# Optimization experiments

Hardware: AMD Instinct MI355X
Metric: run time of the kernel (lower is better)

## Reference

```python
import jax, jax.numpy as jnp
import numpy as np

NEIGHBOR_N = 3


def setup_inputs() -> dict:
    key = jax.random.key(0)
    ks = jax.random.split(key, 4)
    B, D = 8192, 512
    H = D // 2
    sess_emb = jax.random.normal(ks[0], (B, D), dtype=jnp.float32)
    pool_emb = jax.random.normal(ks[1], (1024, D), dtype=jnp.float32)
    # torch Linear default init ~ U(-1/sqrt(fan_in), 1/sqrt(fan_in)); scaled normals ok as baseline
    W1 = jax.random.normal(ks[2], (D, H), dtype=jnp.float32) / np.sqrt(D)
    b1 = jnp.zeros((H,), dtype=jnp.float32)
    W2 = jax.random.normal(ks[3], (H, D), dtype=jnp.float32) / np.sqrt(H)
    b2 = jnp.zeros((D,), dtype=jnp.float32)
    return {"sess_emb": sess_emb, "pool_emb": pool_emb, "W1": W1, "b1": b1, "W2": W2, "b2": b2}


def reference(sess_emb, pool_emb, W1, b1, W2, b2):
    # scoring MLP (dropout = identity in eval mode)
    h = jax.nn.relu(sess_emb @ W1 + b1)          # (B, D/2)
    sess_proj = h @ W2 + b2                       # (B, D)
    # self-similarity and top-k neighbors
    sim_matrix = sess_proj @ sess_proj.T          # (B, B)
    cos_topk, topk_indice = jax.lax.top_k(sim_matrix, NEIGHBOR_N)  # (B, K)
    sess_topk = sess_emb[topk_indice]             # (B, K, D) gather
    cos_topk = jax.nn.softmax(cos_topk, axis=-1)  # (B, K)
    neighbor_sess = jnp.einsum('bk,bkd->bd', cos_topk, sess_topk)  # (B, D)
    return (sess_topk, neighbor_sess, cos_topk)
```

## Files before the change

### kernel.cpp

```cpp
#include <hip/hip_runtime.h>
#include <hip/hip_bf16.h>
#include <math.h>

#define NB 8192
#define DD 512
#define HH 256
#define BM 128
#define BN 256
#define BK 32
#define KT (DD / BK)
#define NCT (NB / BN)
#define NCAND 8

typedef unsigned short ushortT;
typedef __attribute__((ext_vector_type(8))) short bf16x8;
typedef __attribute__((ext_vector_type(4))) float f32x4;

#define AS1(p) ((const __attribute__((address_space(1))) void*)(p))
#define AS3(p) ((__attribute__((address_space(3))) void*)(p))

__device__ __forceinline__ ushortT bf16rne(float f) {
    unsigned u = __float_as_uint(f);
    unsigned r = u + 0x7FFFu + ((u >> 16) & 1u);
    return (ushortT)(r >> 16);
}
__device__ __forceinline__ float bf16tof(ushortT h) {
    return __uint_as_float(((unsigned)h) << 16);
}

__global__ __launch_bounds__(256)
void prep_kernel(const float* __restrict__ sess, const float* __restrict__ W1,
                 const float* __restrict__ W2,
                 ushortT* __restrict__ sess_hi, ushortT* __restrict__ sess_lo,
                 ushortT* __restrict__ w1t_hi, ushortT* __restrict__ w1t_lo,
                 ushortT* __restrict__ w2t_hi, ushortT* __restrict__ w2t_lo) {
    const int b = blockIdx.x, t = threadIdx.x;
    if (b < 2048) {
        size_t i = (size_t)b * 2048 + t * 8;
        float4 f0 = *(const float4*)&sess[i];
        float4 f1 = *(const float4*)&sess[i + 4];
        float f[8] = {f0.x, f0.y, f0.z, f0.w, f1.x, f1.y, f1.z, f1.w};
        unsigned hp[4], lp[4];
#pragma unroll
        for (int j = 0; j < 4; ++j) {
            ushortT h0 = bf16rne(f[2 * j]), h1 = bf16rne(f[2 * j + 1]);
            ushortT l0 = bf16rne(f[2 * j] - bf16tof(h0));
            ushortT l1 = bf16rne(f[2 * j + 1] - bf16tof(h1));
            hp[j] = (unsigned)h0 | ((unsigned)h1 << 16);
            lp[j] = (unsigned)l0 | ((unsigned)l1 << 16);
        }
        *(uint4*)&sess_hi[i] = *(uint4*)hp;
        *(uint4*)&sess_lo[i] = *(uint4*)lp;
    } else if (b < 2112) {
        int o = (b - 2048) * 2048 + t * 8;
        int k = o >> 8, c = o & 255;
        float4 f0 = *(const float4*)&W1[(size_t)k * 256 + c];
        float4 f1 = *(const float4*)&W1[(size_t)k * 256 + c + 4];
        float f[8] = {f0.x, f0.y, f0.z, f0.w, f1.x, f1.y, f1.z, f1.w};
#pragma unroll
        for (int j = 0; j < 8; ++j) {
            ushortT h = bf16rne(f[j]);
            w1t_hi[(size_t)(c + j) * 512 + k] = h;
            w1t_lo[(size_t)(c + j) * 512 + k] = bf16rne(f[j] - bf16tof(h));
        }
    } else {
        int o = (b - 2112) * 2048 + t * 8;
        int k = o >> 9, c = o & 511;
        float4 f0 = *(const float4*)&W2[(size_t)k * 512 + c];
        float4 f1 = *(const float4*)&W2[(size_t)k * 512 + c + 4];
        float f[8] = {f0.x, f0.y, f0.z, f0.w, f1.x, f1.y, f1.z, f1.w};
#pragma unroll
        for (int j = 0; j < 8; ++j) {
            ushortT h = bf16rne(f[j]);
            w2t_hi[(size_t)(c + j) * 256 + k] = h;
            w2t_lo[(size_t)(c + j) * 256 + k] = bf16rne(f[j] - bf16tof(h));
        }
    }
}

template <int KDIM, int NOUT, int EPI>
__global__ __launch_bounds__(256)
void mlp_gemm(const ushortT* __restrict__ Ahi, const ushortT* __restrict__ Alo,
              const ushortT* __restrict__ Bhi, const ushortT* __restrict__ Blo,
              const float* __restrict__ bias,
              ushortT* __restrict__ Ohi, ushortT* __restrict__ Olo,
              float* __restrict__ Of, ushortT* __restrict__ Ob) {
    __shared__ short gsmem[2 * 20480];
    const int KTILES = KDIM / BK;
    const int t = threadIdx.x;
    const int w = t >> 6, l = t & 63;
    const int wr = w >> 1, wc = w & 1;
    const int tx = l & 15, tg = l >> 4;
    const int rb = blockIdx.x * 64;
    const int cb = blockIdx.y * 256;

    const int rin = l >> 2;
    const int tgs = (l & 3) ^ ((rin >> 1) & 3);
    const int loff = tx * BK + ((tg ^ ((tx >> 1) & 3)) << 3);

    f32x4 acc[2][8];
#pragma unroll
    for (int i = 0; i < 2; ++i)
#pragma unroll
        for (int j = 0; j < 8; ++j) acc[i][j] = (f32x4){0.f, 0.f, 0.f, 0.f};

#define GSTAGE(buf, k0v)                                                                     \
    {                                                                                        \
        _Pragma("unroll")                                                                    \
        for (int q = 0; q < 10; ++q) {                                                       \
            int c = w * 10 + q;                                                              \
            const ushortT* src; int row; int lofs;                                           \
            if (c < 4)       { src = Ahi; row = rb + c * 16 + rin;        lofs = 0     + c * 512; }        \
            else if (c < 8)  { src = Alo; row = rb + (c - 4) * 16 + rin;  lofs = 2048  + (c - 4) * 512; }  \
            else if (c < 24) { src = Bhi; row = cb + (c - 8) * 16 + rin;  lofs = 4096  + (c - 8) * 512; }  \
            else             { src = Blo; row = cb + (c - 24) * 16 + rin; lofs = 12288 + (c - 24) * 512; } \
            const ushortT* g = src + (size_t)row * KDIM + (k0v) + tgs * 8;                   \
            __builtin_amdgcn_global_load_lds(AS1(g), AS3(gsmem + (buf) * 20480 + lofs + l * 8), 16, 0, 0); \
        }                                                                                    \
    }

#define GCOMPUTE(kt)                                                                         \
    {                                                                                        \
        const short* Bu = gsmem + ((kt) & 1) * 20480;                                        \
        bf16x8 ah[2], al[2], bh[8], bl[8];                                                   \
        _Pragma("unroll")                                                                    \
        for (int mi = 0; mi < 2; ++mi) {                                                     \
            ah[mi] = *(const bf16x8*)&Bu[0 + (wr * 2 + mi) * 512 + loff];                    \
            al[mi] = *(const bf16x8*)&Bu[2048 + (wr * 2 + mi) * 512 + loff];                 \
        }                                                                                    \
        _Pragma("unroll")                                                                    \
        for (int nj = 0; nj < 8; ++nj) {                                                     \
            bh[nj] = *(const bf16x8*)&Bu[4096 + (wc * 8 + nj) * 512 + loff];                 \
            bl[nj] = *(const bf16x8*)&Bu[12288 + (wc * 8 + nj) * 512 + loff];                \
        }                                                                                    \
        asm volatile("s_waitcnt lgkmcnt(0)" ::: "memory");                                   \
        __builtin_amdgcn_sched_barrier(0);                                                   \
        __builtin_amdgcn_s_barrier();                                                        \
        __builtin_amdgcn_sched_barrier(0);                                                   \
        _Pragma("unroll")                                                                    \
        for (int mi = 0; mi < 2; ++mi)                                                       \
            _Pragma("unroll")                                                                \
            for (int nj = 0; nj < 8; ++nj) {                                                 \
                acc[mi][nj] = __builtin_amdgcn_mfma_f32_16x16x32_bf16(ah[mi], bh[nj], acc[mi][nj], 0, 0, 0); \
                acc[mi][nj] = __builtin_amdgcn_mfma_f32_16x16x32_bf16(ah[mi], bl[nj], acc[mi][nj], 0, 0, 0); \
                acc[mi][nj] = __builtin_amdgcn_mfma_f32_16x16x32_bf16(al[mi], bh[nj], acc[mi][nj], 0, 0, 0); \
            }                                                                                \
    }

    GSTAGE(0, 0);
    for (int kt = 0; kt < KTILES - 1; ++kt) {
        GSTAGE((kt + 1) & 1, (kt + 1) * BK);
        asm volatile("s_waitcnt vmcnt(10)" ::: "memory");
        __builtin_amdgcn_sched_barrier(0);
        __builtin_amdgcn_s_barrier();
        __builtin_amdgcn_sched_barrier(0);
        GCOMPUTE(kt);
    }
    asm volatile("s_waitcnt vmcnt(0)" ::: "memory");
    __builtin_amdgcn_sched_barrier(0);
    __builtin_amdgcn_s_barrier();
    __builtin_amdgcn_sched_barrier(0);
    GCOMPUTE(KTILES - 1);
#undef GSTAGE
#undef GCOMPUTE

#pragma unroll
    for (int mi = 0; mi < 2; ++mi) {
#pragma unroll
        for (int nj = 0; nj < 8; ++nj) {
            int col = cb + wc * 128 + nj * 16 + tx;
            float bv = bias[col];
#pragma unroll
            for (int rr = 0; rr < 4; ++rr) {
                int row = rb + wr * 32 + mi * 16 + tg * 4 + rr;
                float v = acc[mi][nj][rr] + bv;
                if (EPI == 0) {
                    v = fmaxf(v, 0.f);
                    ushortT h = bf16rne(v);
                    Ohi[(size_t)row * NOUT + col] = h;
                    Olo[(size_t)row * NOUT + col] = bf16rne(v - bf16tof(h));
                } else {
                    Of[(size_t)row * NOUT + col] = v;
                    Ob[(size_t)row * NOUT + col] = bf16rne(v);
                }
            }
        }
    }
}

__device__ __forceinline__ void ins3k(unsigned key, unsigned& k0, unsigned& k1, unsigned& k2) {
    bool g0 = key > k0, g1 = key > k1, g2 = key > k2;
    k2 = g1 ? k1 : (g2 ? key : k2);
    k1 = g0 ? k0 : (g1 ? key : k1);
    k0 = g0 ? key : k0;
}
__device__ __forceinline__ void merge3k(unsigned& a0, unsigned& a1, unsigned& a2,
                                        unsigned b0, unsigned b1, unsigned b2) {
    unsigned m0 = a0 > b0 ? a0 : b0;
    bool c0 = a0 > b0;
    unsigned ca1 = c0 ? a1 : b1;
    unsigned cb0 = c0 ? b0 : a0;
    unsigned ca2 = c0 ? a2 : b2;
    unsigned cb1 = c0 ? b1 : a1;
    bool c1 = ca1 > cb0;
    unsigned m1 = c1 ? ca1 : cb0;
    unsigned x = c1 ? ca2 : ca1;
    unsigned y = c1 ? cb0 : cb1;
    unsigned m2 = x > y ? x : y;
    a0 = m0; a1 = m1; a2 = m2;
}

__global__ __launch_bounds__(256)
void sim_mfma_kernel(const short* __restrict__ projb, unsigned* __restrict__ pkeys) {
    __shared__ short smem[2 * BM * BK + 2 * BN * BK];
    short* As = smem;
    short* Bs = smem + 2 * BM * BK;
    unsigned* evu = (unsigned*)smem;

    const int t = threadIdx.x;
    const int w = t >> 6, l = t & 63;
    const int wr = w >> 1, wc = w & 1;
    const int tx = l & 15, tg = l >> 4;
    const int rb = blockIdx.x * BM;
    const int jb = blockIdx.y * BN;

    const int rin = l >> 2;
    const int tgs = (l & 3) ^ ((rin >> 1) & 3);
    const int loff = tx * BK + ((tg ^ ((tx >> 1) & 3)) << 3);

    f32x4 acc[4][8];
#pragma unroll
    for (int i = 0; i < 4; ++i)
#pragma unroll
        for (int j = 0; j < 8; ++j) acc[i][j] = (f32x4){0.f, 0.f, 0.f, 0.f};

#define STAGE(buf, k0)                                                                      \
    {                                                                                       \
        _Pragma("unroll")                                                                   \
        for (int q = 0; q < 6; ++q) {                                                       \
            int c = w * 6 + q;                                                              \
            if (c < 8) {                                                                    \
                const short* g = projb + (size_t)(rb + c * 16 + rin) * DD + (k0) + tgs * 8; \
                __builtin_amdgcn_global_load_lds(AS1(g), AS3(As + (buf) * (BM * BK) + c * 512), 16, 0, 0); \
            } else {                                                                        \
                int cb = c - 8;                                                             \
                const short* g = projb + (size_t)(jb + cb * 16 + rin) * DD + (k0) + tgs * 8; \
                __builtin_amdgcn_global_load_lds(AS1(g), AS3(Bs + (buf) * (BN * BK) + cb * 512), 16, 0, 0); \
            }                                                                               \
        }                                                                                   \
    }

#define COMPUTE(kt)                                                                          \
    {                                                                                        \
        const short* Ab = As + ((kt) & 1) * (BM * BK);                                       \
        const short* Bb = Bs + ((kt) & 1) * (BN * BK);                                       \
        bf16x8 af[4], bfr[8];                                                                \
        _Pragma("unroll")                                                                    \
        for (int mi = 0; mi < 4; ++mi)                                                       \
            af[mi] = *(const bf16x8*)&Ab[(wr * 64 + mi * 16) * BK + loff];                   \
        _Pragma("unroll")                                                                    \
        for (int nj = 0; nj < 8; ++nj)                                                       \
            bfr[nj] = *(const bf16x8*)&Bb[(wc * 128 + nj * 16) * BK + loff];                 \
        asm volatile("s_waitcnt lgkmcnt(0)" ::: "memory");                                   \
        __builtin_amdgcn_sched_barrier(0);                                                   \
        __builtin_amdgcn_s_barrier();                                                        \
        __builtin_amdgcn_sched_barrier(0);                                                   \
        _Pragma("unroll")                                                                    \
        for (int mi = 0; mi < 4; ++mi)                                                       \
            _Pragma("unroll")                                                                \
            for (int nj = 0; nj < 8; ++nj)                                                   \
                acc[mi][nj] = __builtin_amdgcn_mfma_f32_16x16x32_bf16(af[mi], bfr[nj], acc[mi][nj], 0, 0, 0); \
    }

    STAGE(0, 0);
    for (int kt = 0; kt < KT - 1; ++kt) {
        STAGE((kt + 1) & 1, (kt + 1) * BK);
        asm volatile("s_waitcnt vmcnt(6)" ::: "memory");
        __builtin_amdgcn_sched_barrier(0);
        __builtin_amdgcn_s_barrier();
        __builtin_amdgcn_sched_barrier(0);
        COMPUTE(kt);
    }
    asm volatile("s_waitcnt vmcnt(0)" ::: "memory");
    __builtin_amdgcn_sched_barrier(0);
    __builtin_amdgcn_s_barrier();
    __builtin_amdgcn_sched_barrier(0);
    COMPUTE(KT - 1);
#undef STAGE
#undef COMPUTE

    __syncthreads();

    unsigned cinv[8];
#pragma unroll
    for (int nj = 0; nj < 8; ++nj)
        cinv[nj] = 8191u - (unsigned)(jb + wc * 128 + nj * 16 + tx);
#pragma unroll
    for (int mi = 0; mi < 4; ++mi) {
#pragma unroll
        for (int rr = 0; rr < 4; ++rr) {
            unsigned k0 = 0, k1 = 0, k2 = 0;
#pragma unroll
            for (int nj = 0; nj < 8; ++nj) {
                unsigned u = __float_as_uint(acc[mi][nj][rr]);
                unsigned tt = (unsigned)((int)u >> 31) | 0x80000000u;
                unsigned key = ((u ^ tt) & 0xFFFFE000u) | cinv[nj];
                ins3k(key, k0, k1, k2);
            }
#pragma unroll
            for (int s = 1; s <= 2; s <<= 1) {
                unsigned b0 = (unsigned)__shfl_xor((int)k0, s, 64);
                unsigned b1 = (unsigned)__shfl_xor((int)k1, s, 64);
                unsigned b2 = (unsigned)__shfl_xor((int)k2, s, 64);
                merge3k(k0, k1, k2, b0, b1, b2);
            }
            if ((tx & 3) == 0) {
                int lrow = wr * 64 + mi * 16 + tg * 4 + rr;
                unsigned* e = &evu[lrow * 25 + (wc * 4 + (tx >> 2)) * 3];
                e[0] = k0; e[1] = k1; e[2] = k2;
            }
        }
    }
    __syncthreads();
    if (t < BM) {
        unsigned k0 = 0, k1 = 0, k2 = 0;
        const unsigned* e = &evu[t * 25];
#pragma unroll
        for (int s = 0; s < 24; ++s) ins3k(e[s], k0, k1, k2);
        unsigned* pk = pkeys + ((size_t)(rb + t) * NCT + blockIdx.y) * 3;
        pk[0] = k0; pk[1] = k1; pk[2] = k2;
    }
}

__global__ __launch_bounds__(64)
void rerank_out_kernel(const float* __restrict__ proj, const unsigned* __restrict__ pkeys,
                       const float* __restrict__ sess, float* __restrict__ out,
                       float* __restrict__ cos_out) {
    int r = blockIdx.x;
    int t = threadIdx.x;
    unsigned bk[NCAND];
#pragma unroll
    for (int p = 0; p < NCAND; ++p) bk[p] = 0;
    const unsigned* pk = pkeys + (size_t)r * NCT * 3;
    for (int s = 0; s < NCT * 3; ++s) {
        unsigned key = pk[s];
        if (key > bk[NCAND - 1]) {
#pragma unroll
            for (int p = NCAND - 1; p > 0; --p)
                bk[p] = (key > bk[p]) ? ((key > bk[p - 1]) ? bk[p - 1] : key) : bk[p];
            bk[0] = key > bk[0] ? key : bk[0];
        }
    }
    int cj[NCAND];
#pragma unroll
    for (int i = 0; i < NCAND; ++i) cj[i] = 8191 - (int)(bk[i] & 0x1FFFu);

    const float* pr = proj + (size_t)r * DD;
    float myp[8];
#pragma unroll
    for (int k = 0; k < 8; ++k) myp[k] = pr[t * 8 + k];
    double part[NCAND];
#pragma unroll
    for (int i = 0; i < NCAND; ++i) {
        const float* pc = proj + (size_t)cj[i] * DD;
        double s = 0.0;
#pragma unroll
        for (int k = 0; k < 8; ++k) s += (double)myp[k] * (double)pc[t * 8 + k];
        part[i] = s;
    }
#pragma unroll
    for (int i = 0; i < NCAND; ++i) {
#pragma unroll
        for (int s = 1; s < 64; s <<= 1) part[i] += __shfl_xor(part[i], s, 64);
    }
    double bv0 = -1e300, bv1 = -1e300, bv2 = -1e300;
    int bj0 = 0x7fffffff, bj1 = 0x7fffffff, bj2 = 0x7fffffff;
#pragma unroll
    for (int i = 0; i < NCAND; ++i) {
        double v = part[i]; int j = cj[i];
        bool g2 = (v > bv2) || (v == bv2 && j < bj2);
        bool g1 = (v > bv1) || (v == bv1 && j < bj1);
        bool g0 = (v > bv0) || (v == bv0 && j < bj0);
        if (g2) {
            if (g1) {
                if (g0) { bv2 = bv1; bj2 = bj1; bv1 = bv0; bj1 = bj0; bv0 = v; bj0 = j; }
                else    { bv2 = bv1; bj2 = bj1; bv1 = v; bj1 = j; }
            } else      { bv2 = v; bj2 = j; }
        }
    }
    double e1 = exp(bv1 - bv0), e2 = exp(bv2 - bv0);
    double inv = 1.0 / (1.0 + e1 + e2);
    float w0 = (float)inv, w1 = (float)(e1 * inv), w2 = (float)(e2 * inv);
    if (t == 0) {
        cos_out[r * 3 + 0] = w0; cos_out[r * 3 + 1] = w1; cos_out[r * 3 + 2] = w2;
    }
    const float4* s0 = (const float4*)(sess + (size_t)bj0 * DD);
    const float4* s1 = (const float4*)(sess + (size_t)bj1 * DD);
    const float4* s2 = (const float4*)(sess + (size_t)bj2 * DD);
    float4* o = (float4*)(out + (size_t)r * 3 * DD);
    float4* nb = (float4*)(out + (size_t)NB * 3 * DD + (size_t)r * DD);
#pragma unroll
    for (int e = 0; e < 2; ++e) {
        int q = t + e * 64;
        float4 x0 = s0[q], x1 = s1[q], x2 = s2[q];
        o[q] = x0; o[128 + q] = x1; o[256 + q] = x2;
        float4 v;
        v.x = fmaf(w0, x0.x, fmaf(w1, x1.x, w2 * x2.x));
        v.y = fmaf(w0, x0.y, fmaf(w1, x1.y, w2 * x2.y));
        v.z = fmaf(w0, x0.z, fmaf(w1, x1.z, w2 * x2.z));
        v.w = fmaf(w0, x0.w, fmaf(w1, x1.w, w2 * x2.w));
        nb[q] = v;
    }
}

extern "C" void kernel_launch(void* const* d_in, const int* in_sizes, int n_in,
                              void* d_out, int out_size, void* d_ws, size_t ws_size,
                              hipStream_t stream) {
    const float* sess = (const float*)d_in[0];
    const float* W1 = (const float*)d_in[2];
    const float* b1 = (const float*)d_in[3];
    const float* W2 = (const float*)d_in[4];
    const float* b2 = (const float*)d_in[5];
    float* out = (float*)d_out;

    const size_t MBc = 1u << 20;
    char* W = (char*)d_ws;
    float*   proj    = (float*)W;
    ushortT* sess_hi = (ushortT*)W;
    ushortT* sess_lo = sess_hi + (size_t)NB * DD;
    ushortT* projb   = (ushortT*)(W + 16 * MBc);
    ushortT* h_hi    = (ushortT*)(W + 24 * MBc);
    ushortT* h_lo    = (ushortT*)(W + 28 * MBc);
    ushortT* w1t_hi  = (ushortT*)(W + 32 * MBc);
    ushortT* w1t_lo  = w1t_hi + 256 * 512;
    ushortT* w2t_hi  = w1t_lo + 256 * 512;
    ushortT* w2t_lo  = w2t_hi + 512 * 256;
    unsigned* pkeys  = (unsigned*)(W + 33 * MBc);

    float* cos_out = out + (size_t)NB * 3 * DD + (size_t)NB * DD;

    hipLaunchKernelGGL(prep_kernel, dim3(2176), dim3(256), 0, stream,
                       sess, W1, W2, sess_hi, sess_lo, w1t_hi, w1t_lo, w2t_hi, w2t_lo);
    hipLaunchKernelGGL((mlp_gemm<512, 256, 0>), dim3(NB / 64, 1), dim3(256), 0, stream,
                       sess_hi, sess_lo, w1t_hi, w1t_lo, b1, h_hi, h_lo, (float*)nullptr, (ushortT*)nullptr);
    hipLaunchKernelGGL((mlp_gemm<256, 512, 1>), dim3(NB / 64, 2), dim3(256), 0, stream,
                       h_hi, h_lo, w2t_hi, w2t_lo, b2, (ushortT*)nullptr, (ushortT*)nullptr, proj, projb);
    hipLaunchKernelGGL(sim_mfma_kernel, dim3(NB / BM, NCT), dim3(256), 0, stream,
                       (const short*)projb, pkeys);
    hipLaunchKernelGGL(rerank_out_kernel, dim3(NB), dim3(64), 0, stream,
                       proj, pkeys, sess, out, cos_out);
}
```

Measured before the change: 164.2 us.

## Exploit similarity-matrix symmetry: compute upper-triangular tiles and emit transposed top-3 candidates

The self-similarity GEMM now launches only tiles on or above the block diagonal and returns early for the rest. Off-diagonal tiles also reduce each column's top-3 across rows and write those as candidates for the transposed rows, so roughly half the MFMA work is skipped. Candidate keys move to a fixed per-row slot layout that is zeroed by a memset, and the rerank kernel now handles four rows per 256-thread block. The cost is extra per-tile column reduction and shuffles, plus the memset and a doubled candidate buffer to scan in rerank.

After: 235.1 us. +43.2%, slower.

```diff
diff --git a/kernel.cpp b/kernel.cpp
--- a/kernel.cpp
+++ b/kernel.cpp
@@ -9,7 +9,9 @@
 #define BN 256
 #define BK 32
 #define KT (DD / BK)
-#define NCT (NB / BN)
+#define NSLOT 32
+#define NSUB 2
+#define ROWKEYS (NSLOT * NSUB * 3)
 #define NCAND 8
 
 typedef unsigned short ushortT;
@@ -209,20 +211,30 @@
     unsigned m2 = x > y ? x : y;
     a0 = m0; a1 = m1; a2 = m2;
 }
+__device__ __forceinline__ unsigned packkey(float f, unsigned idx) {
+    unsigned u = __float_as_uint(f);
+    unsigned tt = (unsigned)((int)u >> 31) | 0x80000000u;
+    return ((u ^ tt) & 0xFFFFE000u) | (8191u - idx);
+}
 
 __global__ __launch_bounds__(256)
 void sim_mfma_kernel(const short* __restrict__ projb, unsigned* __restrict__ pkeys) {
+    const int ib = blockIdx.x, Jb = blockIdx.y;
+    if (ib > 2 * Jb + 1) return;
+    const bool do_tr = (ib < 2 * Jb);
+
     __shared__ short smem[2 * BM * BK + 2 * BN * BK];
     short* As = smem;
     short* Bs = smem + 2 * BM * BK;
     unsigned* evu = (unsigned*)smem;
+    unsigned* evt = (unsigned*)smem + 3200;
 
     const int t = threadIdx.x;
     const int w = t >> 6, l = t & 63;
     const int wr = w >> 1, wc = w & 1;
     const int tx = l & 15, tg = l >> 4;
-    const int rb = blockIdx.x * BM;
-    const int jb = blockIdx.y * BN;
+    const int rb = ib * BM;
+    const int jb = Jb * BN;
 
     const int rin = l >> 2;
     const int tgs = (l & 3) ^ ((rin >> 1) & 3);
@@ -321,28 +333,64 @@
             }
         }
     }
+
+    if (do_tr) {
+#pragma unroll
+        for (int nj = 0; nj < 8; ++nj) {
+            unsigned k0 = 0, k1 = 0, k2 = 0;
+#pragma unroll
+            for (int mi = 0; mi < 4; ++mi) {
+#pragma unroll
+                for (int rr = 0; rr < 4; ++rr) {
+                    unsigned idx = (unsigned)(rb + wr * 64 + mi * 16 + tg * 4 + rr);
+                    ins3k(packkey(acc[mi][nj][rr], idx), k0, k1, k2);
+                }
+            }
+#pragma unroll
+            for (int s = 16; s <= 32; s <<= 1) {
+                unsigned b0 = (unsigned)__shfl_xor((int)k0, s, 64);
+                unsigned b1 = (unsigned)__shfl_xor((int)k1, s, 64);
+                unsigned b2 = (unsigned)__shfl_xor((int)k2, s, 64);
+                merge3k(k0, k1, k2, b0, b1, b2);
+            }
+            if (tg == 0) {
+                int col = wc * 128 + nj * 16 + tx;
+                unsigned* e = &evt[col * 6 + wr * 3];
+                e[0] = k0; e[1] = k1; e[2] = k2;
+            }
+        }
+    }
     __syncthreads();
+
     if (t < BM) {
         unsigned k0 = 0, k1 = 0, k2 = 0;
         const unsigned* e = &evu[t * 25];
 #pragma unroll
         for (int s = 0; s < 24; ++s) ins3k(e[s], k0, k1, k2);
-        unsigned* pk = pkeys + ((size_t)(rb + t) * NCT + blockIdx.y) * 3;
+        unsigned* pk = pkeys + (size_t)(rb + t) * ROWKEYS + Jb * 6;
         pk[0] = k0; pk[1] = k1; pk[2] = k2;
     }
-}
-
-__global__ __launch_bounds__(64)
+    if (do_tr) {
+        unsigned k0 = 0, k1 = 0, k2 = 0;
+        const unsigned* e = &evt[t * 6];
+#pragma unroll
+        for (int s = 0; s < 6; ++s) ins3k(e[s], k0, k1, k2);
+        unsigned* pk = pkeys + (size_t)(jb + t) * ROWKEYS + (ib >> 1) * 6 + (ib & 1) * 3;
+        pk[0] = k0; pk[1] = k1; pk[2] = k2;
+    }
+}
+
+__global__ __launch_bounds__(256)
 void rerank_out_kernel(const float* __restrict__ proj, const unsigned* __restrict__ pkeys,
                        const float* __restrict__ sess, float* __restrict__ out,
                        float* __restrict__ cos_out) {
-    int r = blockIdx.x;
-    int t = threadIdx.x;
+    int r = blockIdx.x * 4 + (threadIdx.x >> 6);
+    int t = threadIdx.x & 63;
     unsigned bk[NCAND];
 #pragma unroll
     for (int p = 0; p < NCAND; ++p) bk[p] = 0;
-    const unsigned* pk = pkeys + (size_t)r * NCT * 3;
-    for (int s = 0; s < NCT * 3; ++s) {
+    const unsigned* pk = pkeys + (size_t)r * ROWKEYS;
+    for (int s = 0; s < ROWKEYS; ++s) {
         unsigned key = pk[s];
         if (key > bk[NCAND - 1]) {
 #pragma unroll
@@ -435,7 +483,7 @@
     ushortT* w1t_lo  = w1t_hi + 256 * 512;
     ushortT* w2t_hi  = w1t_lo + 256 * 512;
     ushortT* w2t_lo  = w2t_hi + 512 * 256;
-    unsigned* pkeys  = (unsigned*)(W + 33 * MBc);
+    unsigned* pkeys  = (unsigned*)(W + 24 * MBc);
 
     float* cos_out = out + (size_t)NB * 3 * DD + (size_t)NB * DD;
 
@@ -445,8 +493,9 @@
                        sess_hi, sess_lo, w1t_hi, w1t_lo, b1, h_hi, h_lo, (float*)nullptr, (ushortT*)nullptr);
     hipLaunchKernelGGL((mlp_gemm<256, 512, 1>), dim3(NB / 64, 2), dim3(256), 0, stream,
                        h_hi, h_lo, w2t_hi, w2t_lo, b2, (ushortT*)nullptr, (ushortT*)nullptr, proj, projb);
-    hipLaunchKernelGGL(sim_mfma_kernel, dim3(NB / BM, NCT), dim3(256), 0, stream,
+    hipMemsetAsync(pkeys, 0, (size_t)NB * ROWKEYS * sizeof(unsigned), stream);
+    hipLaunchKernelGGL(sim_mfma_kernel, dim3(NB / BM, NB / BN), dim3(256), 0, stream,
                        (const short*)projb, pkeys);
-    hipLaunchKernelGGL(rerank_out_kernel, dim3(NB), dim3(64), 0, stream,
+    hipLaunchKernelGGL(rerank_out_kernel, dim3(NB / 4), dim3(256), 0, stream,
                        proj, pkeys, sess, out, cos_out);
 }
```
